# Optimization experiments

Hardware: AMD Instinct MI355X
Metric: run time of the kernel (lower is better)

The kernel has to match this reference:

```python
import jax, jax.numpy as jnp
import numpy as np

_K = 256  # d_model // 8


def setup_inputs() -> dict:
    key = jax.random.key(0)
    ks = jax.random.split(key, 7)
    B, T, D = 4, 4096, 2048
    x = jax.random.normal(ks[0], (B, T, D), jnp.float32)
    ema_mean = 0.1 * jax.random.normal(ks[1], (D,), jnp.float32)
    # ensure positive variance: ema_sq - ema_mean^2 in [0.5, 1.5]
    ema_sq = ema_mean ** 2 + 0.5 + jax.random.uniform(ks[2], (D,), jnp.float32)
    ema_out = jax.random.normal(ks[3], (D,), jnp.float32)
    log_tau = 0.1 * jax.random.normal(ks[4], (), jnp.float32)
    log_sigma_raw = 0.1 * jax.random.normal(ks[5], (), jnp.float32)
    log_w_raw = 0.1 * jax.random.normal(ks[6], (), jnp.float32)
    return {
        "x": x,
        "ema_mean": ema_mean,
        "ema_sq": ema_sq,
        "ema_out": ema_out,
        "log_tau": log_tau,
        "log_sigma_raw": log_sigma_raw,
        "log_w_raw": log_w_raw,
    }


def reference(x, ema_mean, ema_sq, ema_out, log_tau, log_sigma_raw, log_w_raw):
    tau = jnp.exp(log_tau)
    sigma = jax.nn.softplus(log_sigma_raw) + 0.01
    w = jax.nn.softplus(log_w_raw)

    out = jax.nn.gelu(x, approximate=False)  # F.gelu default = exact erf

    # z-score against EMA stats
    std = jnp.sqrt(jnp.clip(ema_sq - ema_mean ** 2, 1e-6, None))
    z = (x - ema_mean) / std

    # topk |z| over channel dim, gather z, mean of |z_topk|
    _, idx = jax.lax.top_k(jnp.abs(z), _K)          # idx: [B,T,K]
    z_topk = jnp.take_along_axis(z, idx, axis=-1)
    topk_mean = jnp.mean(jnp.abs(z_topk), axis=-1, keepdims=True)  # [B,T,1]
    surp = jnp.tanh(sigma * topk_mean)

    # cosine similarity of gelu output against EMA output direction
    ema_u = ema_out / (jnp.linalg.norm(ema_out) + 1e-8)
    out_n = out / jnp.maximum(
        jnp.linalg.norm(out, axis=-1, keepdims=True), 1e-12
    )  # F.normalize eps
    cos_out = jnp.sum(out_n * ema_u, axis=-1, keepdims=True)  # [B,T,1]

    gate = jnp.exp(-tau * cos_out) * (1.0 + w * surp)
    return out * gate
```

## Files before the change

### kernel.cpp

```cpp
#include <hip/hip_runtime.h>
#include <math.h>

#define D      2048
#define KSEL   256
#define NT     256
#define NBINS  512
#define ROWS   4

typedef float f4 __attribute__((ext_vector_type(4)));
typedef int   i4 __attribute__((ext_vector_type(4)));

__device__ __forceinline__ float fast_gelu(float x) {
    float x2 = x * x;
    float t  = fmaf(x2, -0.0713548162f, -1.5957691216f);
    float e  = __expf(x * t);
    return x * __builtin_amdgcn_rcpf(1.0f + e);
}

template<int CTRL, int RMASK>
__device__ __forceinline__ float dpp_mov_f(float v) {
    int r = __builtin_amdgcn_update_dpp(0, __builtin_bit_cast(int, v),
                                        CTRL, RMASK, 0xf, true);
    return __builtin_bit_cast(float, r);
}
template<int CTRL, int RMASK>
__device__ __forceinline__ int dpp_mov_i(int v) {
    return __builtin_amdgcn_update_dpp(0, v, CTRL, RMASK, 0xf, true);
}
__device__ __forceinline__ float wave_scan_f(float x) {
    x += dpp_mov_f<0x111, 0xf>(x);
    x += dpp_mov_f<0x112, 0xf>(x);
    x += dpp_mov_f<0x114, 0xf>(x);
    x += dpp_mov_f<0x118, 0xf>(x);
    x += dpp_mov_f<0x142, 0xa>(x);
    x += dpp_mov_f<0x143, 0xc>(x);
    return x;
}
__device__ __forceinline__ int wave_scan_i(int x) {
    x += dpp_mov_i<0x111, 0xf>(x);
    x += dpp_mov_i<0x112, 0xf>(x);
    x += dpp_mov_i<0x114, 0xf>(x);
    x += dpp_mov_i<0x118, 0xf>(x);
    x += dpp_mov_i<0x142, 0xa>(x);
    x += dpp_mov_i<0x143, 0xc>(x);
    return x;
}
__device__ __forceinline__ float wave_bcast63_f(float x) {
    int r = __builtin_amdgcn_readlane(__builtin_bit_cast(int, x), 63);
    return __builtin_bit_cast(float, r);
}

__global__ __launch_bounds__(NT) void row_kernel(
    const float* __restrict__ x,
    const float* __restrict__ ema_mean,
    const float* __restrict__ ema_sq,
    const float* __restrict__ ema_out,
    const float* __restrict__ p_log_tau,
    const float* __restrict__ p_log_sigma,
    const float* __restrict__ p_log_w,
    float* __restrict__ out)
{
    __shared__ int   hist[2][NBINS];
    __shared__ float ssred[4];
    __shared__ float red[2][4][2];
    __shared__ float gate_sh[2];

    const int t    = threadIdx.x;
    const int wave = t >> 6;
    const int lane = t & 63;

    const float tau   = __expf(p_log_tau[0]);
    const float sigma = __logf(1.0f + __expf(p_log_sigma[0])) + 0.01f;
    const float w     = __logf(1.0f + __expf(p_log_w[0]));

    f4 m0 = ((const f4*)ema_mean)[t];
    f4 m1 = ((const f4*)ema_mean)[t + NT];
    f4 q0 = ((const f4*)ema_sq)[t];
    f4 q1 = ((const f4*)ema_sq)[t + NT];
    f4 e0 = ((const f4*)ema_out)[t];
    f4 e1 = ((const f4*)ema_out)[t + NT];

    const float mv[8] = {m0.x,m0.y,m0.z,m0.w, m1.x,m1.y,m1.z,m1.w};
    const float qv[8] = {q0.x,q0.y,q0.z,q0.w, q1.x,q1.y,q1.z,q1.w};
    const float ev[8] = {e0.x,e0.y,e0.z,e0.w, e1.x,e1.y,e1.z,e1.w};

    float a_[8], b_[8];
    float ss = 0.f;
#pragma unroll
    for (int j = 0; j < 8; ++j) {
        float v = fmaxf(fmaf(-mv[j], mv[j], qv[j]), 1e-6f);
        a_[j] = 64.0f * __builtin_amdgcn_rsqf(v);
        b_[j] = -mv[j] * a_[j];
        ss = fmaf(ev[j], ev[j], ss);
    }
    ss = wave_scan_f(ss);
    if (lane == 63) ssred[wave] = ss;

    const size_t row0 = (size_t)blockIdx.x * ROWS;
    f4 xa = ((const f4*)(x + row0 * D))[t];
    f4 xb = ((const f4*)(x + row0 * D))[t + NT];

    hist[0][t] = 0;  hist[0][t + NT] = 0;
    hist[1][t] = 0;  hist[1][t + NT] = 0;
    __syncthreads();

    const float inv_nrm =
        1.0f / (sqrtf(ssred[0] + ssred[1] + ssred[2] + ssred[3]) + 1e-8f);
    float u_[8];
#pragma unroll
    for (int j = 0; j < 8; ++j) u_[j] = ev[j] * inv_nrm;

#pragma unroll
    for (int r = 0; r < ROWS; ++r) {
        const int p = r & 1;
        const float xv[8] = {xa.x,xa.y,xa.z,xa.w, xb.x,xb.y,xb.z,xb.w};

        float g[8], av[8];
        float dot = 0.f, nrm = 0.f;
#pragma unroll
        for (int j = 0; j < 8; ++j) {
            float gg = fast_gelu(xv[j]);
            g[j] = gg;
            av[j] = fabsf(fmaf(xv[j], a_[j], b_[j]));
            dot = fmaf(gg, u_[j], dot);
            nrm = fmaf(gg, gg, nrm);
        }

        if (r + 1 < ROWS) {
            const float* xn = x + (row0 + r + 1) * D;
            xa = ((const f4*)xn)[t];
            xb = ((const f4*)xn)[t + NT];
        }

        dot = wave_scan_f(dot);
        nrm = wave_scan_f(nrm);
        if (lane == 63) { red[p][wave][0] = dot; red[p][wave][1] = nrm; }

#pragma unroll
        for (int j = 0; j < 8; ++j) {
            int bin = (int)av[j];
            bin = bin > NBINS - 1 ? NBINS - 1 : bin;
            atomicAdd(&hist[p][(NBINS - 1) - bin], 1);
        }
        __syncthreads();

        if (wave == 0) {
            i4 va = *(const i4*)&hist[p][8 * lane];
            i4 vb = *(const i4*)&hist[p][8 * lane + 4];
            const float base = 511.5f - (float)(8 * lane);
            int c0 = va.x;
            int c1 = c0 + va.y;
            int c2 = c1 + va.z;
            int c3 = c2 + va.w;
            int c4 = c3 + vb.x;
            int c5 = c4 + vb.y;
            int c6 = c5 + vb.z;
            int c7 = c6 + vb.w;
            float w0 = (float)va.x * base;
            float w1 = fmaf((float)va.y, base - 1.0f, w0);
            float w2 = fmaf((float)va.z, base - 2.0f, w1);
            float w3 = fmaf((float)va.w, base - 3.0f, w2);
            float w4 = fmaf((float)vb.x, base - 4.0f, w3);
            float w5 = fmaf((float)vb.y, base - 5.0f, w4);
            float w6 = fmaf((float)vb.z, base - 6.0f, w5);
            float w7 = fmaf((float)vb.w, base - 7.0f, w6);

            int   incl  = wave_scan_i(c7);
            int   excl  = incl - c7;
            float winc  = wave_scan_f(w7);
            float wexcl = winc - w7;

            float ts = 0.f;
            {
                const int   pre[8]  = {0, c0, c1, c2, c3, c4, c5, c6};
                const int   cum[8]  = {c0, c1, c2, c3, c4, c5, c6, c7};
                const float wpre[8] = {0.f, w0, w1, w2, w3, w4, w5, w6};
#pragma unroll
                for (int k = 0; k < 8; ++k) {
                    int s0  = excl + pre[k];
                    int e0x = excl + cum[k];
                    if (s0 < KSEL && e0x >= KSEL)
                        ts = fmaf((float)(KSEL - s0), base - (float)k,
                                  wexcl + wpre[k]);
                }
            }
            ts = wave_bcast63_f(wave_scan_f(ts));

            float dd = red[p][0][0] + red[p][1][0] + red[p][2][0] + red[p][3][0];
            float nn = red[p][0][1] + red[p][1][1] + red[p][2][1] + red[p][3][1];

            const float topk_mean = ts * (1.0f / (64.0f * KSEL));
            const float cosv = dd * __builtin_amdgcn_rsqf(fmaxf(nn, 1e-24f));
            const float yt = sigma * topk_mean;
            const float et = __expf(-2.0f * yt);
            const float th = (1.0f - et) * __builtin_amdgcn_rcpf(1.0f + et);
            const float gate = __expf(-tau * cosv) * fmaf(w, th, 1.0f);
            if (lane == 0) gate_sh[p] = gate;
        } else {
            if (t - 64 < NBINS / 4) {
                ((i4*)&hist[p ^ 1][0])[t - 64] = (i4)0;
            }
        }
        __syncthreads();

        const float gate = gate_sh[p];
        f4 oa, ob;
        oa.x = g[0]*gate; oa.y = g[1]*gate; oa.z = g[2]*gate; oa.w = g[3]*gate;
        ob.x = g[4]*gate; ob.y = g[5]*gate; ob.z = g[6]*gate; ob.w = g[7]*gate;
        f4* outr = (f4*)(out + (row0 + r) * D);
        outr[t]      = oa;
        outr[t + NT] = ob;
    }
}

extern "C" void kernel_launch(void* const* d_in, const int* in_sizes, int n_in,
                              void* d_out, int out_size, void* d_ws, size_t ws_size,
                              hipStream_t stream) {
    (void)n_in; (void)out_size; (void)d_ws; (void)ws_size;
    const float* x         = (const float*)d_in[0];
    const float* ema_mean  = (const float*)d_in[1];
    const float* ema_sq    = (const float*)d_in[2];
    const float* ema_out   = (const float*)d_in[3];
    const float* log_tau   = (const float*)d_in[4];
    const float* log_sigma = (const float*)d_in[5];
    const float* log_w     = (const float*)d_in[6];
    float* out = (float*)d_out;

    const int rows = in_sizes[0] / D;
    row_kernel<<<rows / ROWS, NT, 0, stream>>>(x, ema_mean, ema_sq, ema_out,
                                               log_tau, log_sigma, log_w, out);
}
```

Measured before the change: 47.42 us.

## Process two rows per block concurrently with parallel per-wave histogram scans

Replaces the sequential four-row loop with two rows handled at once per block, loading both rows up front and building both histograms together. Waves 0 and 1 each scan one histogram and compute its gate in parallel, so there are only two barriers per block instead of two per row. The aim is more memory-level parallelism and less serialized barrier and scan latency, at the cost of twice as many blocks (more per-block setup of EMA constants) and higher register pressure.

```diff
diff --git a/kernel.cpp b/kernel.cpp
--- a/kernel.cpp
+++ b/kernel.cpp
@@ -5,7 +5,6 @@
 #define KSEL   256
 #define NT     256
 #define NBINS  512
-#define ROWS   4
 
 typedef float f4 __attribute__((ext_vector_type(4)));
 typedef int   i4 __attribute__((ext_vector_type(4)));
@@ -48,6 +47,60 @@
 __device__ __forceinline__ float wave_bcast63_f(float x) {
     int r = __builtin_amdgcn_readlane(__builtin_bit_cast(int, x), 63);
     return __builtin_bit_cast(float, r);
+}
+
+__device__ __forceinline__ void scan_and_gate(
+    const int* __restrict__ hh, int lane, float tau, float sigma, float w,
+    const float dd, const float nn, float* gate_out)
+{
+    i4 va = *(const i4*)&hh[8 * lane];
+    i4 vb = *(const i4*)&hh[8 * lane + 4];
+    const float base = 511.5f - (float)(8 * lane);
+    int c0 = va.x;
+    int c1 = c0 + va.y;
+    int c2 = c1 + va.z;
+    int c3 = c2 + va.w;
+    int c4 = c3 + vb.x;
+    int c5 = c4 + vb.y;
+    int c6 = c5 + vb.z;
+    int c7 = c6 + vb.w;
+    float w0 = (float)va.x * base;
+    float w1 = fmaf((float)va.y, base - 1.0f, w0);
+    float w2 = fmaf((float)va.z, base - 2.0f, w1);
+    float w3 = fmaf((float)va.w, base - 3.0f, w2);
+    float w4 = fmaf((float)vb.x, base - 4.0f, w3);
+    float w5 = fmaf((float)vb.y, base - 5.0f, w4);
+    float w6 = fmaf((float)vb.z, base - 6.0f, w5);
+    float w7 = fmaf((float)vb.w, base - 7.0f, w6);
+
+    int   incl  = wave_scan_i(c7);
+    int   excl  = incl - c7;
+    float winc  = wave_scan_f(w7);
+    float wexcl = winc - w7;
+
+    float ts = 0.f;
+    {
+        const int   pre[8]  = {0, c0, c1, c2, c3, c4, c5, c6};
+        const int   cum[8]  = {c0, c1, c2, c3, c4, c5, c6, c7};
+        const float wpre[8] = {0.f, w0, w1, w2, w3, w4, w5, w6};
+#pragma unroll
+        for (int k = 0; k < 8; ++k) {
+            int s0  = excl + pre[k];
+            int e0x = excl + cum[k];
+            if (s0 < KSEL && e0x >= KSEL)
+                ts = fmaf((float)(KSEL - s0), base - (float)k,
+                          wexcl + wpre[k]);
+        }
+    }
+    ts = wave_bcast63_f(wave_scan_f(ts));
+
+    const float topk_mean = ts * (1.0f / (64.0f * KSEL));
+    const float cosv = dd * __builtin_amdgcn_rsqf(fmaxf(nn, 1e-24f));
+    const float yt = sigma * topk_mean;
+    const float et = __expf(-2.0f * yt);
+    const float th = (1.0f - et) * __builtin_amdgcn_rcpf(1.0f + et);
+    const float gate = __expf(-tau * cosv) * fmaf(w, th, 1.0f);
+    if (lane == 0) *gate_out = gate;
 }
 
 __global__ __launch_bounds__(NT) void row_kernel(
@@ -80,6 +133,12 @@
     f4 e0 = ((const f4*)ema_out)[t];
     f4 e1 = ((const f4*)ema_out)[t + NT];
 
+    const size_t row0 = (size_t)blockIdx.x * 2;
+    f4 xa0 = ((const f4*)(x + row0 * D))[t];
+    f4 xb0 = ((const f4*)(x + row0 * D))[t + NT];
+    f4 xa1 = ((const f4*)(x + (row0 + 1) * D))[t];
+    f4 xb1 = ((const f4*)(x + (row0 + 1) * D))[t + NT];
+
     const float mv[8] = {m0.x,m0.y,m0.z,m0.w, m1.x,m1.y,m1.z,m1.w};
     const float qv[8] = {q0.x,q0.y,q0.z,q0.w, q1.x,q1.y,q1.z,q1.w};
     const float ev[8] = {e0.x,e0.y,e0.z,e0.w, e1.x,e1.y,e1.z,e1.w};
@@ -96,10 +155,6 @@
     ss = wave_scan_f(ss);
     if (lane == 63) ssred[wave] = ss;
 
-    const size_t row0 = (size_t)blockIdx.x * ROWS;
-    f4 xa = ((const f4*)(x + row0 * D))[t];
-    f4 xb = ((const f4*)(x + row0 * D))[t + NT];
-
     hist[0][t] = 0;  hist[0][t + NT] = 0;
     hist[1][t] = 0;  hist[1][t + NT] = 0;
     __syncthreads();
@@ -110,107 +165,66 @@
 #pragma unroll
     for (int j = 0; j < 8; ++j) u_[j] = ev[j] * inv_nrm;
 
-#pragma unroll
-    for (int r = 0; r < ROWS; ++r) {
-        const int p = r & 1;
-        const float xv[8] = {xa.x,xa.y,xa.z,xa.w, xb.x,xb.y,xb.z,xb.w};
-
-        float g[8], av[8];
-        float dot = 0.f, nrm = 0.f;
-#pragma unroll
-        for (int j = 0; j < 8; ++j) {
-            float gg = fast_gelu(xv[j]);
-            g[j] = gg;
-            av[j] = fabsf(fmaf(xv[j], a_[j], b_[j]));
-            dot = fmaf(gg, u_[j], dot);
-            nrm = fmaf(gg, gg, nrm);
-        }
-
-        if (r + 1 < ROWS) {
-            const float* xn = x + (row0 + r + 1) * D;
-            xa = ((const f4*)xn)[t];
-            xb = ((const f4*)xn)[t + NT];
-        }
-
-        dot = wave_scan_f(dot);
-        nrm = wave_scan_f(nrm);
-        if (lane == 63) { red[p][wave][0] = dot; red[p][wave][1] = nrm; }
-
-#pragma unroll
-        for (int j = 0; j < 8; ++j) {
-            int bin = (int)av[j];
-            bin = bin > NBINS - 1 ? NBINS - 1 : bin;
-            atomicAdd(&hist[p][(NBINS - 1) - bin], 1);
-        }
-        __syncthreads();
-
-        if (wave == 0) {
-            i4 va = *(const i4*)&hist[p][8 * lane];
-            i4 vb = *(const i4*)&hist[p][8 * lane + 4];
-            const float base = 511.5f - (float)(8 * lane);
-            int c0 = va.x;
-            int c1 = c0 + va.y;
-            int c2 = c1 + va.z;
-            int c3 = c2 + va.w;
-            int c4 = c3 + vb.x;
-            int c5 = c4 + vb.y;
-            int c6 = c5 + vb.z;
-            int c7 = c6 + vb.w;
-            float w0 = (float)va.x * base;
-            float w1 = fmaf((float)va.y, base - 1.0f, w0);
-            float w2 = fmaf((float)va.z, base - 2.0f, w1);
-            float w3 = fmaf((float)va.w, base - 3.0f, w2);
-            float w4 = fmaf((float)vb.x, base - 4.0f, w3);
-            float w5 = fmaf((float)vb.y, base - 5.0f, w4);
-            float w6 = fmaf((float)vb.z, base - 6.0f, w5);
-            float w7 = fmaf((float)vb.w, base - 7.0f, w6);
-
-            int   incl  = wave_scan_i(c7);
-            int   excl  = incl - c7;
-            float winc  = wave_scan_f(w7);
-            float wexcl = winc - w7;
-
-            float ts = 0.f;
-            {
-                const int   pre[8]  = {0, c0, c1, c2, c3, c4, c5, c6};
-                const int   cum[8]  = {c0, c1, c2, c3, c4, c5, c6, c7};
-                const float wpre[8] = {0.f, w0, w1, w2, w3, w4, w5, w6};
-#pragma unroll
-                for (int k = 0; k < 8; ++k) {
-                    int s0  = excl + pre[k];
-                    int e0x = excl + cum[k];
-                    if (s0 < KSEL && e0x >= KSEL)
-                        ts = fmaf((float)(KSEL - s0), base - (float)k,
-                                  wexcl + wpre[k]);
-                }
-            }
-            ts = wave_bcast63_f(wave_scan_f(ts));
-
-            float dd = red[p][0][0] + red[p][1][0] + red[p][2][0] + red[p][3][0];
-            float nn = red[p][0][1] + red[p][1][1] + red[p][2][1] + red[p][3][1];
-
-            const float topk_mean = ts * (1.0f / (64.0f * KSEL));
-            const float cosv = dd * __builtin_amdgcn_rsqf(fmaxf(nn, 1e-24f));
-            const float yt = sigma * topk_mean;
-            const float et = __expf(-2.0f * yt);
-            const float th = (1.0f - et) * __builtin_amdgcn_rcpf(1.0f + et);
-            const float gate = __expf(-tau * cosv) * fmaf(w, th, 1.0f);
-            if (lane == 0) gate_sh[p] = gate;
-        } else {
-            if (t - 64 < NBINS / 4) {
-                ((i4*)&hist[p ^ 1][0])[t - 64] = (i4)0;
-            }
-        }
-        __syncthreads();
-
-        const float gate = gate_sh[p];
-        f4 oa, ob;
-        oa.x = g[0]*gate; oa.y = g[1]*gate; oa.z = g[2]*gate; oa.w = g[3]*gate;
-        ob.x = g[4]*gate; ob.y = g[5]*gate; ob.z = g[6]*gate; ob.w = g[7]*gate;
-        f4* outr = (f4*)(out + (row0 + r) * D);
-        outr[t]      = oa;
-        outr[t + NT] = ob;
-    }
+    const float xv0[8] = {xa0.x,xa0.y,xa0.z,xa0.w, xb0.x,xb0.y,xb0.z,xb0.w};
+    const float xv1[8] = {xa1.x,xa1.y,xa1.z,xa1.w, xb1.x,xb1.y,xb1.z,xb1.w};
+
+    float g0[8], g1[8], av0[8], av1[8];
+    float dot0 = 0.f, nrm0 = 0.f, dot1 = 0.f, nrm1 = 0.f;
+#pragma unroll
+    for (int j = 0; j < 8; ++j) {
+        float ga = fast_gelu(xv0[j]);
+        float gb = fast_gelu(xv1[j]);
+        g0[j] = ga;  g1[j] = gb;
+        av0[j] = fabsf(fmaf(xv0[j], a_[j], b_[j]));
+        av1[j] = fabsf(fmaf(xv1[j], a_[j], b_[j]));
+        dot0 = fmaf(ga, u_[j], dot0);
+        nrm0 = fmaf(ga, ga, nrm0);
+        dot1 = fmaf(gb, u_[j], dot1);
+        nrm1 = fmaf(gb, gb, nrm1);
+    }
+
+    dot0 = wave_scan_f(dot0);
+    nrm0 = wave_scan_f(nrm0);
+    dot1 = wave_scan_f(dot1);
+    nrm1 = wave_scan_f(nrm1);
+    if (lane == 63) {
+        red[0][wave][0] = dot0; red[0][wave][1] = nrm0;
+        red[1][wave][0] = dot1; red[1][wave][1] = nrm1;
+    }
+
+#pragma unroll
+    for (int j = 0; j < 8; ++j) {
+        int b0 = (int)av0[j];  b0 = b0 > NBINS - 1 ? NBINS - 1 : b0;
+        int b1 = (int)av1[j];  b1 = b1 > NBINS - 1 ? NBINS - 1 : b1;
+        atomicAdd(&hist[0][(NBINS - 1) - b0], 1);
+        atomicAdd(&hist[1][(NBINS - 1) - b1], 1);
+    }
+    __syncthreads();
+
+    if (wave == 0) {
+        float dd = red[0][0][0] + red[0][1][0] + red[0][2][0] + red[0][3][0];
+        float nn = red[0][0][1] + red[0][1][1] + red[0][2][1] + red[0][3][1];
+        scan_and_gate(&hist[0][0], lane, tau, sigma, w, dd, nn, &gate_sh[0]);
+    } else if (wave == 1) {
+        float dd = red[1][0][0] + red[1][1][0] + red[1][2][0] + red[1][3][0];
+        float nn = red[1][0][1] + red[1][1][1] + red[1][2][1] + red[1][3][1];
+        scan_and_gate(&hist[1][0], lane, tau, sigma, w, dd, nn, &gate_sh[1]);
+    }
+    __syncthreads();
+
+    const float gateA = gate_sh[0];
+    const float gateB = gate_sh[1];
+    f4 oa, ob;
+    oa.x = g0[0]*gateA; oa.y = g0[1]*gateA; oa.z = g0[2]*gateA; oa.w = g0[3]*gateA;
+    ob.x = g0[4]*gateA; ob.y = g0[5]*gateA; ob.z = g0[6]*gateA; ob.w = g0[7]*gateA;
+    f4* outr0 = (f4*)(out + row0 * D);
+    outr0[t]      = oa;
+    outr0[t + NT] = ob;
+    oa.x = g1[0]*gateB; oa.y = g1[1]*gateB; oa.z = g1[2]*gateB; oa.w = g1[3]*gateB;
+    ob.x = g1[4]*gateB; ob.y = g1[5]*gateB; ob.z = g1[6]*gateB; ob.w = g1[7]*gateB;
+    f4* outr1 = (f4*)(out + (row0 + 1) * D);
+    outr1[t]      = oa;
+    outr1[t + NT] = ob;
 }
 
 extern "C" void kernel_launch(void* const* d_in, const int* in_sizes, int n_in,
@@ -227,6 +241,6 @@
     float* out = (float*)d_out;
 
     const int rows = in_sizes[0] / D;
-    row_kernel<<<rows / ROWS, NT, 0, stream>>>(x, ema_mean, ema_sq, ema_out,
-                                               log_tau, log_sigma, log_w, out);
-}
+    row_kernel<<<rows / 2, NT, 0, stream>>>(x, ema_mean, ema_sq, ema_out,
+                                            log_tau, log_sigma, log_w, out);
+}
```

Result: faster. 45.31 us (-4.5%).
